# Performance work log

Measured on AMD Instinct MI355X. Metric: run time of the kernel, lower is better.

Reference implementation:

```python
import jax, jax.numpy as jnp
import numpy as np
from jax import lax

K = 3          # kernel size
STRIDE = 1
PAD = 1
DIL = 1


def conv2d(x, w, b, stride, pad):
    y = lax.conv_general_dilated(
        x, w, (stride, stride), [(pad, pad), (pad, pad)],
        dimension_numbers=('NCHW', 'OIHW', 'NCHW'))
    return y + b[None, :, None, None]


def deform_conv2d(x, offset, mask, weight, bias):
    # x: [B,C,H,W]; offset: [B,2*K*K,Ho,Wo] (channel 2i = y_i, 2i+1 = x_i);
    # mask: [B,K*K,Ho,Wo]; weight: [Cout,C,K,K]  (deformable_groups=1, groups=1)
    B, C, H, W = x.shape
    Ho, Wo = offset.shape[2], offset.shape[3]
    KK = K * K
    off = offset.reshape(B, KK, 2, Ho, Wo)
    off_y, off_x = off[:, :, 0], off[:, :, 1]          # [B,KK,Ho,Wo]

    ky, kx = jnp.meshgrid(jnp.arange(K), jnp.arange(K), indexing='ij')
    ky, kx = ky.ravel(), kx.ravel()                    # [KK]
    base_y = (jnp.arange(Ho) * STRIDE - PAD)[None, :, None] + (ky * DIL)[:, None, None]
    base_x = (jnp.arange(Wo) * STRIDE - PAD)[None, None, :] + (kx * DIL)[:, None, None]
    py = base_y[None].astype(x.dtype) + off_y          # [B,KK,Ho,Wo]
    px = base_x[None].astype(x.dtype) + off_x

    y0 = jnp.floor(py)
    x0 = jnp.floor(px)
    ly = py - y0
    lx = px - x0
    y0i = y0.astype(jnp.int32)
    x0i = x0.astype(jnp.int32)
    y1i = y0i + 1
    x1i = x0i + 1

    x_flat = x.reshape(B, C, H * W)

    def gather(yi, xi):
        valid = (yi >= 0) & (yi < H) & (xi >= 0) & (xi < W)
        idx = jnp.clip(yi, 0, H - 1) * W + jnp.clip(xi, 0, W - 1)
        v = jax.vmap(lambda xb, ib: xb[:, ib])(x_flat, idx.reshape(B, -1))
        v = v.reshape(B, C, KK, Ho, Wo)
        return v * valid[:, None].astype(x.dtype)

    w00 = ((1 - ly) * (1 - lx))[:, None]
    w01 = ((1 - ly) * lx)[:, None]
    w10 = (ly * (1 - lx))[:, None]
    w11 = (ly * lx)[:, None]
    samp = (w00 * gather(y0i, x0i) + w01 * gather(y0i, x1i)
            + w10 * gather(y1i, x0i) + w11 * gather(y1i, x1i))  # [B,C,KK,Ho,Wo]

    mod = samp * mask[:, None]                          # modulated samples
    wr = weight.reshape(weight.shape[0], C, KK)
    out = jnp.einsum('ocp,bcphw->bohw', wr, mod)
    return out + bias[None, :, None, None]


def setup_inputs() -> dict:
    key = jax.random.key(0)
    k1, k2, k3, k4, k5 = jax.random.split(key, 5)
    B, Cin, Cout, H, W = 4, 64, 128, 128, 128
    x = jax.random.normal(k1, (B, Cin, H, W), dtype=jnp.float32)
    # offset/mask conv: 3*K*K channels (o1, o2, mask). Zero-init in the source;
    # small random values here so nonzero offsets exercise the gather.
    offset_w = jax.random.normal(k2, (3 * K * K, Cin, K, K), dtype=jnp.float32) * 0.01
    offset_b = jax.random.normal(k3, (3 * K * K,), dtype=jnp.float32) * 0.01
    weight = jax.random.normal(k4, (Cout, Cin, K, K), dtype=jnp.float32) * (1.0 / np.sqrt(Cin * K * K))
    bias = jax.random.normal(k5, (Cout,), dtype=jnp.float32) * 0.01
    return {'x': x, 'offset_w': offset_w, 'offset_b': offset_b, 'weight': weight, 'bias': bias}


def reference(x, offset_w, offset_b, weight, bias):
    out = conv2d(x, offset_w, offset_b, STRIDE, PAD)    # [B,3*KK,Ho,Wo]
    o1, o2, m = jnp.split(out, 3, axis=1)
    offset = jnp.concatenate([o1, o2], axis=1)          # [B,2*KK,Ho,Wo]
    mask = jax.nn.sigmoid(m)                            # [B,KK,Ho,Wo]
    return deform_conv2d(x, offset, mask, weight, bias)
```

## Files before the change

kernel.cpp:

```cpp
#include <hip/hip_runtime.h>
#include <math.h>

#define HH   128
#define WW   128
#define HWP  16384
#define CIN  64
#define COUT 128

typedef float  f32x4  __attribute__((ext_vector_type(4)));
typedef short  short8 __attribute__((ext_vector_type(8)));

#define WBF_B   ((size_t)0)
#define OWBF_B  ((size_t)147456)
#define XT_B    ((size_t)221184)
#define WS_NEED ((size_t)8609792)

__device__ inline unsigned short f2bf(float f) {
    unsigned u = __builtin_bit_cast(unsigned, f);
    return (unsigned short)((u + 0x7FFFu + ((u >> 16) & 1u)) >> 16);
}

__global__ __launch_bounds__(256) void k_prep(const float* __restrict__ x,
                                              const float* __restrict__ wgt,
                                              const float* __restrict__ ow,
                                              unsigned short* __restrict__ xt,
                                              unsigned short* __restrict__ wbf,
                                              unsigned short* __restrict__ owbf) {
    int t = threadIdx.x;
    if (blockIdx.x < 2048) {
        int cgrp = t & 7, px = t >> 3;
        int pix = blockIdx.x * 32 + px;
        int b = pix >> 14, hw = pix & 16383;
        const float* xp = x + (size_t)b * CIN * HWP + (size_t)(cgrp * 8) * HWP + hw;
        unsigned pk[4];
#pragma unroll
        for (int d = 0; d < 4; ++d) {
            float lo = xp[(size_t)(2 * d) * HWP];
            float hi = xp[(size_t)(2 * d + 1) * HWP];
            pk[d] = (unsigned)f2bf(lo) | ((unsigned)f2bf(hi) << 16);
        }
        *(uint4*)(xt + (size_t)pix * 64 + cgrp * 8) = *(uint4*)pk;
    } else {
        int tid = (blockIdx.x - 2048) * 256 + t;
        {
            int oc = tid / 576;
            int r  = tid - oc * 576;
            int kk = r >> 6;
            int c  = r & 63;
            wbf[tid] = f2bf(wgt[((size_t)oc * CIN + c) * 9 + kk]);
        }
        if (tid < 32 * 576) {
            int oc  = tid / 576;
            int r   = tid - oc * 576;
            int tap = r >> 6;
            int c   = r & 63;
            owbf[tid] = (oc < 27) ? f2bf(ow[((size_t)oc * CIN + c) * 9 + tap]) : 0;
        }
    }
}

__global__ __launch_bounds__(256) void k_fused_v2(const unsigned short* __restrict__ xt,
                                                  const unsigned short* __restrict__ wbf,
                                                  const unsigned short* __restrict__ owbf,
                                                  const float* __restrict__ ob,
                                                  const float* __restrict__ bias,
                                                  float* __restrict__ out) {
    __shared__ __align__(16) char smem[11648];
    char*  mbase  = smem;
    float* meta_s = (float*)(smem + 8192);

    int blk0 = blockIdx.x;
    int blk  = (blk0 & 7) * 256 + (blk0 >> 3);
    int b   = blk >> 9;
    int rem = blk & 511;
    int h   = rem >> 2;
    int w0  = (rem & 3) << 5;
    int t   = threadIdx.x;

    int p1 = t >> 3;
    int cg = t & 7;
    int l  = t & 63;
    int wid = t >> 6;
    int lm = l & 15, lk = l >> 4;

    const unsigned short* xbt = xt + (size_t)b * HWP * 64;

    int ocf = wid >> 1, pxf = wid & 1;
    int spx = pxf * 16 + lm;
    f32x4 sacc = {0.f, 0.f, 0.f, 0.f};
    const unsigned short* sab = owbf + (size_t)(ocf * 16 + lm) * 576 + lk * 8;

#pragma unroll
    for (int tap = 0; tap < 9; ++tap) {
        int ky = tap / 3, kx = tap % 3;
        int yy = h - 1 + ky;
        int xx = w0 - 1 + kx + spx;
        bool vld = (yy >= 0) && (yy < HH) && (xx >= 0) && (xx < WW);
        int yc = min(max(yy, 0), HH - 1), xc = min(max(xx, 0), WW - 1);
        const unsigned short* bp = xbt + (size_t)(yc * WW + xc) * 64 + lk * 8;
#pragma unroll
        for (int ch = 0; ch < 2; ++ch) {
            short8 a = *(const short8*)(sab + tap * 64 + ch * 32);
            uint4 v = *(const uint4*)(bp + ch * 32);
            v.x = vld ? v.x : 0u;  v.y = vld ? v.y : 0u;
            v.z = vld ? v.z : 0u;  v.w = vld ? v.w : 0u;
            sacc = __builtin_amdgcn_mfma_f32_16x16x32_bf16(a, __builtin_bit_cast(short8, v), sacc, 0, 0, 0);
        }
    }
#pragma unroll
    for (int r = 0; r < 4; ++r) {
        int oc = ocf * 16 + lk * 4 + r;
        if (oc < 27) {
            float v = sacc[r] + ob[oc];
            if (oc < 18) {
                meta_s[(oc & 1) * 288 + (oc >> 1) * 32 + spx] = v;
            } else {
                meta_s[2 * 288 + (oc - 18) * 32 + spx] = 1.f / (1.f + expf(-v));
            }
        }
    }
    __syncthreads();

    f32x4 acc00 = {0.f,0.f,0.f,0.f};
    f32x4 acc01 = {0.f,0.f,0.f,0.f};
    f32x4 acc10 = {0.f,0.f,0.f,0.f};
    f32x4 acc11 = {0.f,0.f,0.f,0.f};

    const unsigned short* arow0 = wbf + (size_t)(wid * 32 + lm) * 576 + lk * 8;
    const unsigned short* arow1 = arow0 + 16 * 576;

    int pA = lm, pB = lm + 16;
    int rbA = pA * 128, rbB = pB * 128;
    int swA = pA & 7,   swB = pB & 7;

    uint4 cc00, cc01, cc10, cc11;
    float cw00, cw01, cw10, cw11;

    const unsigned short* xbc = xbt + cg * 8;

#define PREF_CORNERS(KK) do {                                                  \
      int ky_ = (KK) / 3, kx_ = (KK) % 3;                                      \
      float offy = meta_s[(KK) * 32 + p1];                                     \
      float offx = meta_s[288 + (KK) * 32 + p1];                               \
      float msk  = meta_s[576 + (KK) * 32 + p1];                               \
      float py = (float)(h - 1 + ky_) + offy;                                  \
      float px = (float)(w0 + p1 - 1 + kx_) + offx;                            \
      float y0f = floorf(py), x0f = floorf(px);                                \
      float ly = py - y0f, lx = px - x0f;                                      \
      int y0 = (int)y0f, x0i = (int)x0f;                                       \
      int y1 = y0 + 1, x1 = x0i + 1;                                           \
      bool vy0 = (y0 >= 0) && (y0 < HH);                                       \
      bool vy1 = (y1 >= 0) && (y1 < HH);                                       \
      bool vx0 = (x0i >= 0) && (x0i < WW);                                     \
      bool vx1 = (x1 >= 0) && (x1 < WW);                                       \
      int yc0 = min(max(y0, 0), HH - 1), yc1 = min(max(y1, 0), HH - 1);        \
      int xc0 = min(max(x0i, 0), WW - 1), xc1 = min(max(x1, 0), WW - 1);       \
      cw00 = (1.f - ly) * (1.f - lx) * ((vy0 && vx0) ? msk : 0.f);             \
      cw01 = (1.f - ly) * lx         * ((vy0 && vx1) ? msk : 0.f);             \
      cw10 = ly * (1.f - lx)         * ((vy1 && vx0) ? msk : 0.f);             \
      cw11 = ly * lx                 * ((vy1 && vx1) ? msk : 0.f);             \
      cc00 = *(const uint4*)(xbc + (size_t)(yc0 * WW + xc0) * 64);             \
      cc01 = *(const uint4*)(xbc + (size_t)(yc0 * WW + xc1) * 64);             \
      cc10 = *(const uint4*)(xbc + (size_t)(yc1 * WW + xc0) * 64);             \
      cc11 = *(const uint4*)(xbc + (size_t)(yc1 * WW + xc1) * 64);             \
    } while (0)

    PREF_CORNERS(0);

#pragma unroll
    for (int kk = 0; kk < 9; ++kk) {
        const int cur = kk & 1;
        {
            char* wdst = mbase + cur * 4096;
            unsigned pk[4];
#pragma unroll
            for (int d = 0; d < 4; ++d) {
                unsigned u0 = (&cc00.x)[d], u1 = (&cc01.x)[d];
                unsigned u2 = (&cc10.x)[d], u3 = (&cc11.x)[d];
                float lo = cw00 * __builtin_bit_cast(float, u0 << 16)
                         + cw01 * __builtin_bit_cast(float, u1 << 16)
                         + cw10 * __builtin_bit_cast(float, u2 << 16)
                         + cw11 * __builtin_bit_cast(float, u3 << 16);
                float hi = cw00 * __builtin_bit_cast(float, u0 & 0xFFFF0000u)
                         + cw01 * __builtin_bit_cast(float, u1 & 0xFFFF0000u)
                         + cw10 * __builtin_bit_cast(float, u2 & 0xFFFF0000u)
                         + cw11 * __builtin_bit_cast(float, u3 & 0xFFFF0000u);
                pk[d] = (unsigned)f2bf(lo) | ((unsigned)f2bf(hi) << 16);
            }
            *(uint4*)(wdst + p1 * 128 + (((unsigned)(cg ^ (p1 & 7))) << 4)) = *(uint4*)pk;
        }

        if (kk < 8) PREF_CORNERS(kk + 1);

        asm volatile("s_waitcnt lgkmcnt(0)" ::: "memory");
        __builtin_amdgcn_s_barrier();
        __builtin_amdgcn_sched_barrier(0);

        const char* rb = mbase + cur * 4096;
#pragma unroll
        for (int sstep = 0; sstep < 2; ++sstep) {
            short8 a0 = *(const short8*)(arow0 + kk * 64 + sstep * 32);
            short8 a1 = *(const short8*)(arow1 + kk * 64 + sstep * 32);
            int kb = sstep * 4 + lk;
            short8 b0 = *(const short8*)(rb + rbA + ((kb ^ swA) << 4));
            short8 b1 = *(const short8*)(rb + rbB + ((kb ^ swB) << 4));
            acc00 = __builtin_amdgcn_mfma_f32_16x16x32_bf16(a0, b0, acc00, 0, 0, 0);
            acc01 = __builtin_amdgcn_mfma_f32_16x16x32_bf16(a0, b1, acc01, 0, 0, 0);
            acc10 = __builtin_amdgcn_mfma_f32_16x16x32_bf16(a1, b0, acc10, 0, 0, 0);
            acc11 = __builtin_amdgcn_mfma_f32_16x16x32_bf16(a1, b1, acc11, 0, 0, 0);
        }
    }
#undef PREF_CORNERS

    size_t outb = (size_t)b * COUT * HWP + (size_t)h * WW + w0;
#pragma unroll
    for (int of = 0; of < 2; ++of) {
        f32x4 aP = of ? acc10 : acc00;
        f32x4 aQ = of ? acc11 : acc01;
        int ocb = wid * 32 + of * 16 + lk * 4;
#pragma unroll
        for (int r = 0; r < 4; ++r) {
            int oc = ocb + r;
            float bi = bias[oc];
            out[outb + (size_t)oc * HWP + pA] = aP[r] + bi;
            out[outb + (size_t)oc * HWP + pB] = aQ[r] + bi;
        }
    }
}

__global__ __launch_bounds__(256) void k_fused_v1(const float* __restrict__ x,
                                                  const unsigned short* __restrict__ wbf,
                                                  const unsigned short* __restrict__ owbf,
                                                  const float* __restrict__ ob,
                                                  const float* __restrict__ bias,
                                                  float* __restrict__ out) {
    __shared__ __align__(16) char smem[16768];
    char*  ctx    = smem;
    char*  mbase  = smem;
    float* meta_s = (float*)(smem + 13312);

    int blk = blockIdx.x;
    int b   = blk >> 9;
    int rem = blk & 511;
    int h   = rem >> 2;
    int w0  = (rem & 3) << 5;
    int t   = threadIdx.x;

    int p1 = t & 31;
    int cg = t >> 5;
    int l  = t & 63;
    int wid = t >> 6;
    int lm = l & 15, lk = l >> 4;

    const float* xb = x + (size_t)b * CIN * HWP;

#pragma unroll
    for (int c = 0; c < 4; ++c) {
        int j = c * 256 + t;
        if (j < 816) {
            int g   = j / 34;
            int px  = j - g * 34;
            int row = g >> 3;
            int cgj = g & 7;
            int yy = h - 1 + row;
            int xx = w0 - 1 + px;
            bool vld = (yy >= 0) && (yy < HH) && (xx >= 0) && (xx < WW);
            int  sidx = vld ? (yy * WW + xx) : 0;
            float s[8];
#pragma unroll
            for (int i = 0; i < 8; ++i)
                s[i] = vld ? xb[(size_t)(cgj * 8 + i) * HWP + sidx] : 0.f;
            uint4 pk;
            pk.x = (unsigned)f2bf(s[0]) | ((unsigned)f2bf(s[1]) << 16);
            pk.y = (unsigned)f2bf(s[2]) | ((unsigned)f2bf(s[3]) << 16);
            pk.z = (unsigned)f2bf(s[4]) | ((unsigned)f2bf(s[5]) << 16);
            pk.w = (unsigned)f2bf(s[6]) | ((unsigned)f2bf(s[7]) << 16);
            *(uint4*)(ctx + (row * 34 + px) * 128 + ((cgj ^ (px & 7)) << 4)) = pk;
        }
    }
    __syncthreads();

    int ocf = wid >> 1, pxf = wid & 1;
    int spx = pxf * 16 + lm;
    f32x4 sacc = {0.f, 0.f, 0.f, 0.f};
    const unsigned short* sab = owbf + (size_t)(ocf * 16 + lm) * 576 + lk * 8;

#pragma unroll
    for (int tap = 0; tap < 9; ++tap) {
        int ky = tap / 3, kx = tap % 3;
        int cpx = kx + spx;
        int crb = (ky * 34 + cpx) * 128;
        int csw = cpx & 7;
#pragma unroll
        for (int ch = 0; ch < 2; ++ch) {
            short8 a  = *(const short8*)(sab + tap * 64 + ch * 32);
            int kb = ch * 4 + lk;
            short8 bf = *(const short8*)(ctx + crb + (((unsigned)(kb ^ csw)) << 4));
            sacc = __builtin_amdgcn_mfma_f32_16x16x32_bf16(a, bf, sacc, 0, 0, 0);
        }
    }
#pragma unroll
    for (int r = 0; r < 4; ++r) {
        int oc = ocf * 16 + lk * 4 + r;
        if (oc < 27) {
            float v = sacc[r] + ob[oc];
            if (oc < 18) {
                meta_s[(oc & 1) * 288 + (oc >> 1) * 32 + spx] = v;
            } else {
                meta_s[2 * 288 + (oc - 18) * 32 + spx] = 1.f / (1.f + expf(-v));
            }
        }
    }
    __syncthreads();

    f32x4 acc00 = {0.f,0.f,0.f,0.f};
    f32x4 acc01 = {0.f,0.f,0.f,0.f};
    f32x4 acc10 = {0.f,0.f,0.f,0.f};
    f32x4 acc11 = {0.f,0.f,0.f,0.f};

    const unsigned short* arow0 = wbf + (size_t)(wid * 32 + lm) * 576 + lk * 8;
    const unsigned short* arow1 = arow0 + 16 * 576;

    int pA = lm, pB = lm + 16;
    int rbA = pA * 128, rbB = pB * 128;
    int swA = pA & 7,   swB = pB & 7;

    float  cw00, cw01, cw10, cw11;
    float  cc00[8], cc01[8], cc10[8], cc11[8];
    short8 na0[2], na1[2];

#define PREF_CORNERS(KK) do {                                                  \
      int ky = (KK) / 3, kx = (KK) % 3;                                        \
      float offy = meta_s[(KK) * 32 + p1];                                     \
      float offx = meta_s[288 + (KK) * 32 + p1];                               \
      float msk  = meta_s[576 + (KK) * 32 + p1];                               \
      float py = (float)(h - 1 + ky) + offy;                                   \
      float px = (float)(w0 + p1 - 1 + kx) + offx;                             \
      float y0f = floorf(py), x0f = floorf(px);                                \
      float ly = py - y0f, lx = px - x0f;                                      \
      int y0 = (int)y0f, x0i = (int)x0f;                                       \
      int y1 = y0 + 1, x1 = x0i + 1;                                           \
      bool vy0 = (y0 >= 0) && (y0 < HH);                                       \
      bool vy1 = (y1 >= 0) && (y1 < HH);                                       \
      bool vx0 = (x0i >= 0) && (x0i < WW);                                     \
      bool vx1 = (x1 >= 0) && (x1 < WW);                                       \
      int yc0 = min(max(y0, 0), HH - 1), yc1 = min(max(y1, 0), HH - 1);        \
      int xc0 = min(max(x0i, 0), WW - 1), xc1 = min(max(x1, 0), WW - 1);       \
      cw00 = (1.f - ly) * (1.f - lx) * ((vy0 && vx0) ? msk : 0.f);             \
      cw01 = (1.f - ly) * lx         * ((vy0 && vx1) ? msk : 0.f);             \
      cw10 = ly * (1.f - lx)         * ((vy1 && vx0) ? msk : 0.f);             \
      cw11 = ly * lx                 * ((vy1 && vx1) ? msk : 0.f);             \
      int idx00 = yc0 * WW + xc0, idx01 = yc0 * WW + xc1;                      \
      int idx10 = yc1 * WW + xc0, idx11 = yc1 * WW + xc1;                      \
      const float* basec = xb + (size_t)(cg * 8) * HWP;                        \
      _Pragma("unroll")                                                        \
      for (int i = 0; i < 8; ++i) {                                            \
        const float* bc = basec + (size_t)i * HWP;                             \
        cc00[i] = bc[idx00]; cc01[i] = bc[idx01];                              \
        cc10[i] = bc[idx10]; cc11[i] = bc[idx11];                              \
      }                                                                        \
    } while (0)

#define PREF_AFRAG(KK) do {                                                    \
      na0[0] = *(const short8*)(arow0 + (KK) * 64);                            \
      na0[1] = *(const short8*)(arow0 + (KK) * 64 + 32);                       \
      na1[0] = *(const short8*)(arow1 + (KK) * 64);                            \
      na1[1] = *(const short8*)(arow1 + (KK) * 64 + 32);                       \
    } while (0)

    PREF_CORNERS(0);
    PREF_AFRAG(0);

#pragma unroll
    for (int kk = 0; kk < 9; ++kk) {
        {
            char* wdst = mbase + (kk & 1) * 4096;
            float s[8];
#pragma unroll
            for (int i = 0; i < 8; ++i)
                s[i] = cw00 * cc00[i] + cw01 * cc01[i]
                     + cw10 * cc10[i] + cw11 * cc11[i];
            uint4 pk;
            pk.x = (unsigned)f2bf(s[0]) | ((unsigned)f2bf(s[1]) << 16);
            pk.y = (unsigned)f2bf(s[2]) | ((unsigned)f2bf(s[3]) << 16);
            pk.z = (unsigned)f2bf(s[4]) | ((unsigned)f2bf(s[5]) << 16);
            pk.w = (unsigned)f2bf(s[6]) | ((unsigned)f2bf(s[7]) << 16);
            *(uint4*)(wdst + p1 * 128 + (((unsigned)(cg ^ (p1 & 7))) << 4)) = pk;
        }
        if (kk < 8) PREF_CORNERS(kk + 1);
        asm volatile("s_waitcnt lgkmcnt(0)" ::: "memory");
        __builtin_amdgcn_s_barrier();
        __builtin_amdgcn_sched_barrier(0);
        const char* rb = mbase + (kk & 1) * 4096;
#pragma unroll
        for (int sstep = 0; sstep < 2; ++sstep) {
            short8 a0 = na0[sstep];
            short8 a1 = na1[sstep];
            int kb = sstep * 4 + lk;
            short8 b0 = *(const short8*)(rb + rbA + ((kb ^ swA) << 4));
            short8 b1 = *(const short8*)(rb + rbB + ((kb ^ swB) << 4));
            acc00 = __builtin_amdgcn_mfma_f32_16x16x32_bf16(a0, b0, acc00, 0, 0, 0);
            acc01 = __builtin_amdgcn_mfma_f32_16x16x32_bf16(a0, b1, acc01, 0, 0, 0);
            acc10 = __builtin_amdgcn_mfma_f32_16x16x32_bf16(a1, b0, acc10, 0, 0, 0);
            acc11 = __builtin_amdgcn_mfma_f32_16x16x32_bf16(a1, b1, acc11, 0, 0, 0);
        }
        if (kk < 8) PREF_AFRAG(kk + 1);
    }
#undef PREF_CORNERS
#undef PREF_AFRAG

    size_t outb = (size_t)b * COUT * HWP + (size_t)h * WW + w0;
#pragma unroll
    for (int of = 0; of < 2; ++of) {
        f32x4 aP = of ? acc10 : acc00;
        f32x4 aQ = of ? acc11 : acc01;
        int ocb = wid * 32 + of * 16 + lk * 4;
#pragma unroll
        for (int r = 0; r < 4; ++r) {
            int oc = ocb + r;
            float bi = bias[oc];
            out[outb + (size_t)oc * HWP + pA] = aP[r] + bi;
            out[outb + (size_t)oc * HWP + pB] = aQ[r] + bi;
        }
    }
}

extern "C" void kernel_launch(void* const* d_in, const int* in_sizes, int n_in,
                              void* d_out, int out_size, void* d_ws, size_t ws_size,
                              hipStream_t stream) {
    const float* x    = (const float*)d_in[0];
    const float* ow   = (const float*)d_in[1];
    const float* ob   = (const float*)d_in[2];
    const float* wgt  = (const float*)d_in[3];
    const float* bias = (const float*)d_in[4];
    float* out = (float*)d_out;
    char* ws = (char*)d_ws;

    unsigned short* wbf  = (unsigned short*)(ws + WBF_B);
    unsigned short* owbf = (unsigned short*)(ws + OWBF_B);
    unsigned short* xt   = (unsigned short*)(ws + XT_B);

    if (ws_size >= WS_NEED) {
        hipLaunchKernelGGL(k_prep, dim3(2336), dim3(256), 0, stream,
                           x, wgt, ow, xt, wbf, owbf);
        hipLaunchKernelGGL(k_fused_v2, dim3(2048), dim3(256), 0, stream,
                           xt, wbf, owbf, ob, bias, out);
    } else {
        hipLaunchKernelGGL(k_prep, dim3(2336), dim3(256), 0, stream,
                           x, wgt, ow, xt, wbf, owbf);
        hipLaunchKernelGGL(k_fused_v1, dim3(2048), dim3(256), 0, stream,
                           x, wbf, owbf, ob, bias, out);
    }
}
```

Measured before the change: 92.34 us.

## Split offset/mask conv into separate kernel writing fp16 metadata to workspace

Moves the offset/mask convolution out of the fused deformable-conv kernel into a new k_offc kernel. It processes two rows per block and computes all 27 channels per warp, then writes fp16 offsets and sigmoid masks to workspace. The main kernel loads this metadata instead of recomputing the small MFMA conv, which removes per-block conv work and its gather latency. The cost is an extra launch, fp16 precision loss on offsets, and extra global traffic. It also swizzles the prep block order, drops the fp32 fallback kernel, and removes the A-fragment prefetch in the main loop.

Measured after the change: 86.12 us. 6.7% less time.

```diff
diff --git a/kernel.cpp b/kernel.cpp
--- a/kernel.cpp
+++ b/kernel.cpp
@@ -1,4 +1,5 @@
 #include <hip/hip_runtime.h>
+#include <hip/hip_fp16.h>
 #include <math.h>
 
 #define HH   128
@@ -10,10 +11,12 @@
 typedef float  f32x4  __attribute__((ext_vector_type(4)));
 typedef short  short8 __attribute__((ext_vector_type(8)));
 
-#define WBF_B   ((size_t)0)
-#define OWBF_B  ((size_t)147456)
-#define XT_B    ((size_t)221184)
-#define WS_NEED ((size_t)8609792)
+#define WBF_B    ((size_t)0)
+#define OWBF_B   ((size_t)147456)
+#define XT_B     ((size_t)221184)
+#define META_B   ((size_t)8609792)
+#define WS_NEED  ((size_t)8609792)
+#define WS_NEED3 ((size_t)12148736)
 
 __device__ inline unsigned short f2bf(float f) {
     unsigned u = __builtin_bit_cast(unsigned, f);
@@ -28,8 +31,10 @@
                                               unsigned short* __restrict__ owbf) {
     int t = threadIdx.x;
     if (blockIdx.x < 2048) {
+        int bid  = blockIdx.x;
+        int bid2 = (bid & 7) * 256 + (bid >> 3);
         int cgrp = t & 7, px = t >> 3;
-        int pix = blockIdx.x * 32 + px;
+        int pix = bid2 * 32 + px;
         int b = pix >> 14, hw = pix & 16383;
         const float* xp = x + (size_t)b * CIN * HWP + (size_t)(cgrp * 8) * HWP + hw;
         unsigned pk[4];
@@ -59,12 +64,77 @@
     }
 }
 
-__global__ __launch_bounds__(256) void k_fused_v2(const unsigned short* __restrict__ xt,
-                                                  const unsigned short* __restrict__ wbf,
-                                                  const unsigned short* __restrict__ owbf,
-                                                  const float* __restrict__ ob,
-                                                  const float* __restrict__ bias,
-                                                  float* __restrict__ out) {
+__global__ __launch_bounds__(256) void k_offc(const unsigned short* __restrict__ xt,
+                                              const unsigned short* __restrict__ owbf,
+                                              const float* __restrict__ ob,
+                                              __half* __restrict__ meta_h) {
+    int blk0 = blockIdx.x;
+    int blk  = (blk0 & 7) * 128 + (blk0 >> 3);
+    int b    = blk >> 8;
+    int rem  = blk & 255;
+    int h    = (rem >> 2) * 2;
+    int w0   = (rem & 3) << 5;
+    int t    = threadIdx.x;
+    int l    = t & 63;
+    int wid  = t >> 6;
+    int lm   = l & 15, lk = l >> 4;
+
+    int r   = wid >> 1;
+    int pxf = wid & 1;
+    h += r;
+    int spx = pxf * 16 + lm;
+
+    const unsigned short* xbt = xt + (size_t)b * HWP * 64;
+    f32x4 acc0 = {0.f,0.f,0.f,0.f};
+    f32x4 acc1 = {0.f,0.f,0.f,0.f};
+    const unsigned short* sab0 = owbf + (size_t)lm * 576 + lk * 8;
+    const unsigned short* sab1 = sab0 + 16 * 576;
+
+#pragma unroll
+    for (int tap = 0; tap < 9; ++tap) {
+        int ky = tap / 3, kx = tap % 3;
+        int yy = h - 1 + ky;
+        int xx = w0 - 1 + kx + spx;
+        bool vld = (yy >= 0) && (yy < HH) && (xx >= 0) && (xx < WW);
+        int yc = min(max(yy, 0), HH - 1), xc = min(max(xx, 0), WW - 1);
+        const unsigned short* bp = xbt + (size_t)(yc * WW + xc) * 64 + lk * 8;
+        uint4 v0 = *(const uint4*)bp;
+        uint4 v1 = *(const uint4*)(bp + 32);
+        if (!vld) { v0 = uint4{0,0,0,0}; v1 = uint4{0,0,0,0}; }
+        short8 b0 = __builtin_bit_cast(short8, v0);
+        short8 b1 = __builtin_bit_cast(short8, v1);
+        short8 a00 = *(const short8*)(sab0 + tap * 64);
+        short8 a01 = *(const short8*)(sab0 + tap * 64 + 32);
+        short8 a10 = *(const short8*)(sab1 + tap * 64);
+        short8 a11 = *(const short8*)(sab1 + tap * 64 + 32);
+        acc0 = __builtin_amdgcn_mfma_f32_16x16x32_bf16(a00, b0, acc0, 0, 0, 0);
+        acc0 = __builtin_amdgcn_mfma_f32_16x16x32_bf16(a01, b1, acc0, 0, 0, 0);
+        acc1 = __builtin_amdgcn_mfma_f32_16x16x32_bf16(a10, b0, acc1, 0, 0, 0);
+        acc1 = __builtin_amdgcn_mfma_f32_16x16x32_bf16(a11, b1, acc1, 0, 0, 0);
+    }
+
+    int hw = h * WW + w0 + spx;
+#pragma unroll
+    for (int q = 0; q < 4; ++q) {
+        int oc0 = lk * 4 + q;
+        float v0 = acc0[q] + ob[oc0];
+        meta_h[((size_t)((oc0 & 1) * 9 + (oc0 >> 1)) * 4 + b) * HWP + hw] = __float2half(v0);
+        int oc1 = 16 + lk * 4 + q;
+        if (oc1 < 27) {
+            float v1 = acc1[q] + ob[oc1];
+            int comp, kk;
+            if (oc1 < 18) { comp = oc1 & 1; kk = oc1 >> 1; }
+            else          { comp = 2; kk = oc1 - 18; v1 = 1.f / (1.f + expf(-v1)); }
+            meta_h[((size_t)(comp * 9 + kk) * 4 + b) * HWP + hw] = __float2half(v1);
+        }
+    }
+}
+
+__global__ __launch_bounds__(256) void k_main(const unsigned short* __restrict__ xt,
+                                              const unsigned short* __restrict__ wbf,
+                                              const __half* __restrict__ meta_h,
+                                              const float* __restrict__ bias,
+                                              float* __restrict__ out) {
     __shared__ __align__(16) char smem[11648];
     char*  mbase  = smem;
     float* meta_s = (float*)(smem + 8192);
@@ -85,38 +155,14 @@
 
     const unsigned short* xbt = xt + (size_t)b * HWP * 64;
 
-    int ocf = wid >> 1, pxf = wid & 1;
-    int spx = pxf * 16 + lm;
-    f32x4 sacc = {0.f, 0.f, 0.f, 0.f};
-    const unsigned short* sab = owbf + (size_t)(ocf * 16 + lm) * 576 + lk * 8;
-
-#pragma unroll
-    for (int tap = 0; tap < 9; ++tap) {
-        int ky = tap / 3, kx = tap % 3;
-        int yy = h - 1 + ky;
-        int xx = w0 - 1 + kx + spx;
-        bool vld = (yy >= 0) && (yy < HH) && (xx >= 0) && (xx < WW);
-        int yc = min(max(yy, 0), HH - 1), xc = min(max(xx, 0), WW - 1);
-        const unsigned short* bp = xbt + (size_t)(yc * WW + xc) * 64 + lk * 8;
-#pragma unroll
-        for (int ch = 0; ch < 2; ++ch) {
-            short8 a = *(const short8*)(sab + tap * 64 + ch * 32);
-            uint4 v = *(const uint4*)(bp + ch * 32);
-            v.x = vld ? v.x : 0u;  v.y = vld ? v.y : 0u;
-            v.z = vld ? v.z : 0u;  v.w = vld ? v.w : 0u;
-            sacc = __builtin_amdgcn_mfma_f32_16x16x32_bf16(a, __builtin_bit_cast(short8, v), sacc, 0, 0, 0);
-        }
-    }
-#pragma unroll
-    for (int r = 0; r < 4; ++r) {
-        int oc = ocf * 16 + lk * 4 + r;
-        if (oc < 27) {
-            float v = sacc[r] + ob[oc];
-            if (oc < 18) {
-                meta_s[(oc & 1) * 288 + (oc >> 1) * 32 + spx] = v;
-            } else {
-                meta_s[2 * 288 + (oc - 18) * 32 + spx] = 1.f / (1.f + expf(-v));
-            }
+    {
+        int base_hw = h * WW + w0;
+        for (int j = t; j < 864; j += 256) {
+            int px = j & 31;
+            int ck = j >> 5;
+            float v = __half2float(meta_h[((size_t)ck * 4 + b) * HWP + base_hw + px]);
+            int comp = ck / 9, kk = ck - comp * 9;
+            meta_s[comp * 288 + kk * 32 + px] = v;
         }
     }
     __syncthreads();
@@ -189,13 +235,10 @@
             }
             *(uint4*)(wdst + p1 * 128 + (((unsigned)(cg ^ (p1 & 7))) << 4)) = *(uint4*)pk;
         }
-
         if (kk < 8) PREF_CORNERS(kk + 1);
-
         asm volatile("s_waitcnt lgkmcnt(0)" ::: "memory");
         __builtin_amdgcn_s_barrier();
         __builtin_amdgcn_sched_barrier(0);
-
         const char* rb = mbase + cur * 4096;
 #pragma unroll
         for (int sstep = 0; sstep < 2; ++sstep) {
@@ -219,66 +262,40 @@
         f32x4 aQ = of ? acc11 : acc01;
         int ocb = wid * 32 + of * 16 + lk * 4;
 #pragma unroll
-        for (int r = 0; r < 4; ++r) {
-            int oc = ocb + r;
+        for (int q = 0; q < 4; ++q) {
+            int oc = ocb + q;
             float bi = bias[oc];
-            out[outb + (size_t)oc * HWP + pA] = aP[r] + bi;
-            out[outb + (size_t)oc * HWP + pB] = aQ[r] + bi;
-        }
-    }
-}
-
-__global__ __launch_bounds__(256) void k_fused_v1(const float* __restrict__ x,
+            out[outb + (size_t)oc * HWP + pA] = aP[q] + bi;
+            out[outb + (size_t)oc * HWP + pB] = aQ[q] + bi;
+        }
+    }
+}
+
+__global__ __launch_bounds__(256) void k_fused_v2(const unsigned short* __restrict__ xt,
                                                   const unsigned short* __restrict__ wbf,
                                                   const unsigned short* __restrict__ owbf,
                                                   const float* __restrict__ ob,
                                                   const float* __restrict__ bias,
                                                   float* __restrict__ out) {
-    __shared__ __align__(16) char smem[16768];
-    char*  ctx    = smem;
+    __shared__ __align__(16) char smem[11648];
     char*  mbase  = smem;
-    float* meta_s = (float*)(smem + 13312);
-
-    int blk = blockIdx.x;
+    float* meta_s = (float*)(smem + 8192);
+
+    int blk0 = blockIdx.x;
+    int blk  = (blk0 & 7) * 256 + (blk0 >> 3);
     int b   = blk >> 9;
     int rem = blk & 511;
     int h   = rem >> 2;
     int w0  = (rem & 3) << 5;
     int t   = threadIdx.x;
 
-    int p1 = t & 31;
-    int cg = t >> 5;
+    int p1 = t >> 3;
+    int cg = t & 7;
     int l  = t & 63;
     int wid = t >> 6;
     int lm = l & 15, lk = l >> 4;
 
-    const float* xb = x + (size_t)b * CIN * HWP;
-
-#pragma unroll
-    for (int c = 0; c < 4; ++c) {
-        int j = c * 256 + t;
-        if (j < 816) {
-            int g   = j / 34;
-            int px  = j - g * 34;
-            int row = g >> 3;
-            int cgj = g & 7;
-            int yy = h - 1 + row;
-            int xx = w0 - 1 + px;
-            bool vld = (yy >= 0) && (yy < HH) && (xx >= 0) && (xx < WW);
-            int  sidx = vld ? (yy * WW + xx) : 0;
-            float s[8];
-#pragma unroll
-            for (int i = 0; i < 8; ++i)
-                s[i] = vld ? xb[(size_t)(cgj * 8 + i) * HWP + sidx] : 0.f;
-            uint4 pk;
-            pk.x = (unsigned)f2bf(s[0]) | ((unsigned)f2bf(s[1]) << 16);
-            pk.y = (unsigned)f2bf(s[2]) | ((unsigned)f2bf(s[3]) << 16);
-            pk.z = (unsigned)f2bf(s[4]) | ((unsigned)f2bf(s[5]) << 16);
-            pk.w = (unsigned)f2bf(s[6]) | ((unsigned)f2bf(s[7]) << 16);
-            *(uint4*)(ctx + (row * 34 + px) * 128 + ((cgj ^ (px & 7)) << 4)) = pk;
-        }
-    }
-    __syncthreads();
+    const unsigned short* xbt = xt + (size_t)b * HWP * 64;
 
     int ocf = wid >> 1, pxf = wid & 1;
     int spx = pxf * 16 + lm;
@@ -288,22 +305,25 @@
 #pragma unroll
     for (int tap = 0; tap < 9; ++tap) {
         int ky = tap / 3, kx = tap % 3;
-        int cpx = kx + spx;
-        int crb = (ky * 34 + cpx) * 128;
-        int csw = cpx & 7;
+        int yy = h - 1 + ky;
+        int xx = w0 - 1 + kx + spx;
+        bool vld = (yy >= 0) && (yy < HH) && (xx >= 0) && (xx < WW);
+        int yc = min(max(yy, 0), HH - 1), xc = min(max(xx, 0), WW - 1);
+        const unsigned short* bp = xbt + (size_t)(yc * WW + xc) * 64 + lk * 8;
 #pragma unroll
         for (int ch = 0; ch < 2; ++ch) {
-            short8 a  = *(const short8*)(sab + tap * 64 + ch * 32);
-            int kb = ch * 4 + lk;
-            short8 bf = *(const short8*)(ctx + crb + (((unsigned)(kb ^ csw)) << 4));
-            sacc = __builtin_amdgcn_mfma_f32_16x16x32_bf16(a, bf, sacc, 0, 0, 0);
-        }
-    }
-#pragma unroll
-    for (int r = 0; r < 4; ++r) {
-        int oc = ocf * 16 + lk * 4 + r;
+            short8 a = *(const short8*)(sab + tap * 64 + ch * 32);
+            uint4 v = *(const uint4*)(bp + ch * 32);
+            v.x = vld ? v.x : 0u;  v.y = vld ? v.y : 0u;
+            v.z = vld ? v.z : 0u;  v.w = vld ? v.w : 0u;
+            sacc = __builtin_amdgcn_mfma_f32_16x16x32_bf16(a, __builtin_bit_cast(short8, v), sacc, 0, 0, 0);
+        }
+    }
+#pragma unroll
+    for (int q = 0; q < 4; ++q) {
+        int oc = ocf * 16 + lk * 4 + q;
         if (oc < 27) {
-            float v = sacc[r] + ob[oc];
+            float v = sacc[q] + ob[oc];
             if (oc < 18) {
                 meta_s[(oc & 1) * 288 + (oc >> 1) * 32 + spx] = v;
             } else {
@@ -325,17 +345,18 @@
     int rbA = pA * 128, rbB = pB * 128;
     int swA = pA & 7,   swB = pB & 7;
 
-    float  cw00, cw01, cw10, cw11;
-    float  cc00[8], cc01[8], cc10[8], cc11[8];
-    short8 na0[2], na1[2];
+    uint4 cc00, cc01, cc10, cc11;
+    float cw00, cw01, cw10, cw11;
+
+    const unsigned short* xbc = xbt + cg * 8;
 
 #define PREF_CORNERS(KK) do {                                                  \
-      int ky = (KK) / 3, kx = (KK) % 3;                                        \
+      int ky_ = (KK) / 3, kx_ = (KK) % 3;                                      \
       float offy = meta_s[(KK) * 32 + p1];                                     \
       float offx = meta_s[288 + (KK) * 32 + p1];                               \
       float msk  = meta_s[576 + (KK) * 32 + p1];                               \
-      float py = (float)(h - 1 + ky) + offy;                                   \
-      float px = (float)(w0 + p1 - 1 + kx) + offx;                             \
+      float py = (float)(h - 1 + ky_) + offy;                                  \
+      float px = (float)(w0 + p1 - 1 + kx_) + offx;                            \
       float y0f = floorf(py), x0f = floorf(px);                                \
       float ly = py - y0f, lx = px - x0f;                                      \
       int y0 = (int)y0f, x0i = (int)x0f;                                       \
@@ -350,52 +371,45 @@
       cw01 = (1.f - ly) * lx         * ((vy0 && vx1) ? msk : 0.f);             \
       cw10 = ly * (1.f - lx)         * ((vy1 && vx0) ? msk : 0.f);             \
       cw11 = ly * lx                 * ((vy1 && vx1) ? msk : 0.f);             \
-      int idx00 = yc0 * WW + xc0, idx01 = yc0 * WW + xc1;                      \
-      int idx10 = yc1 * WW + xc0, idx11 = yc1 * WW + xc1;                      \
-      const float* basec = xb + (size_t)(cg * 8) * HWP;                        \
-      _Pragma("unroll")                                                        \
-      for (int i = 0; i < 8; ++i) {                                            \
-        const float* bc = basec + (size_t)i * HWP;                             \
-        cc00[i] = bc[idx00]; cc01[i] = bc[idx01];                              \
-        cc10[i] = bc[idx10]; cc11[i] = bc[idx11];                              \
-      }                                                                        \
+      cc00 = *(const uint4*)(xbc + (size_t)(yc0 * WW + xc0) * 64);             \
+      cc01 = *(const uint4*)(xbc + (size_t)(yc0 * WW + xc1) * 64);             \
+      cc10 = *(const uint4*)(xbc + (size_t)(yc1 * WW + xc0) * 64);             \
+      cc11 = *(const uint4*)(xbc + (size_t)(yc1 * WW + xc1) * 64);             \
     } while (0)
 
-#define PREF_AFRAG(KK) do {                                                    \
-      na0[0] = *(const short8*)(arow0 + (KK) * 64);                            \
-      na0[1] = *(const short8*)(arow0 + (KK) * 64 + 32);                       \
-      na1[0] = *(const short8*)(arow1 + (KK) * 64);                            \
-      na1[1] = *(const short8*)(arow1 + (KK) * 64 + 32);                       \
-    } while (0)
-
     PREF_CORNERS(0);
-    PREF_AFRAG(0);
 
 #pragma unroll
     for (int kk = 0; kk < 9; ++kk) {
+        const int cur = kk & 1;
         {
-            char* wdst = mbase + (kk & 1) * 4096;
-            float s[8];
-#pragma unroll
-            for (int i = 0; i < 8; ++i)
-                s[i] = cw00 * cc00[i] + cw01 * cc01[i]
-                     + cw10 * cc10[i] + cw11 * cc11[i];
-            uint4 pk;
-            pk.x = (unsigned)f2bf(s[0]) | ((unsigned)f2bf(s[1]) << 16);
-            pk.y = (unsigned)f2bf(s[2]) | ((unsigned)f2bf(s[3]) << 16);
-            pk.z = (unsigned)f2bf(s[4]) | ((unsigned)f2bf(s[5]) << 16);
-            pk.w = (unsigned)f2bf(s[6]) | ((unsigned)f2bf(s[7]) << 16);
-            *(uint4*)(wdst + p1 * 128 + (((unsigned)(cg ^ (p1 & 7))) << 4)) = pk;
+            char* wdst = mbase + cur * 4096;
+            unsigned pk[4];
+#pragma unroll
+            for (int d = 0; d < 4; ++d) {
+                unsigned u0 = (&cc00.x)[d], u1 = (&cc01.x)[d];
+                unsigned u2 = (&cc10.x)[d], u3 = (&cc11.x)[d];
+                float lo = cw00 * __builtin_bit_cast(float, u0 << 16)
+                         + cw01 * __builtin_bit_cast(float, u1 << 16)
+                         + cw10 * __builtin_bit_cast(float, u2 << 16)
+                         + cw11 * __builtin_bit_cast(float, u3 << 16);
+                float hi = cw00 * __builtin_bit_cast(float, u0 & 0xFFFF0000u)
+                         + cw01 * __builtin_bit_cast(float, u1 & 0xFFFF0000u)
+                         + cw10 * __builtin_bit_cast(float, u2 & 0xFFFF0000u)
+                         + cw11 * __builtin_bit_cast(float, u3 & 0xFFFF0000u);
+                pk[d] = (unsigned)f2bf(lo) | ((unsigned)f2bf(hi) << 16);
+            }
+            *(uint4*)(wdst + p1 * 128 + (((unsigned)(cg ^ (p1 & 7))) << 4)) = *(uint4*)pk;
         }
         if (kk < 8) PREF_CORNERS(kk + 1);
         asm volatile("s_waitcnt lgkmcnt(0)" ::: "memory");
         __builtin_amdgcn_s_barrier();
         __builtin_amdgcn_sched_barrier(0);
-        const char* rb = mbase + (kk & 1) * 4096;
+        const char* rb = mbase + cur * 4096;
 #pragma unroll
         for (int sstep = 0; sstep < 2; ++sstep) {
-            short8 a0 = na0[sstep];
-            short8 a1 = na1[sstep];
+            short8 a0 = *(const short8*)(arow0 + kk * 64 + sstep * 32);
+            short8 a1 = *(const short8*)(arow1 + kk * 64 + sstep * 32);
             int kb = sstep * 4 + lk;
             short8 b0 = *(const short8*)(rb + rbA + ((kb ^ swA) << 4));
             short8 b1 = *(const short8*)(rb + rbB + ((kb ^ swB) << 4));
@@ -404,10 +418,8 @@
             acc10 = __builtin_amdgcn_mfma_f32_16x16x32_bf16(a1, b0, acc10, 0, 0, 0);
             acc11 = __builtin_amdgcn_mfma_f32_16x16x32_bf16(a1, b1, acc11, 0, 0, 0);
         }
-        if (kk < 8) PREF_AFRAG(kk + 1);
     }
 #undef PREF_CORNERS
-#undef PREF_AFRAG
 
     size_t outb = (size_t)b * COUT * HWP + (size_t)h * WW + w0;
 #pragma unroll
@@ -416,11 +428,11 @@
         f32x4 aQ = of ? acc11 : acc01;
         int ocb = wid * 32 + of * 16 + lk * 4;
 #pragma unroll
-        for (int r = 0; r < 4; ++r) {
-            int oc = ocb + r;
+        for (int q = 0; q < 4; ++q) {
+            int oc = ocb + q;
             float bi = bias[oc];
-            out[outb + (size_t)oc * HWP + pA] = aP[r] + bi;
-            out[outb + (size_t)oc * HWP + pB] = aQ[r] + bi;
+            out[outb + (size_t)oc * HWP + pA] = aP[q] + bi;
+            out[outb + (size_t)oc * HWP + pB] = aQ[q] + bi;
         }
     }
 }
@@ -439,16 +451,17 @@
     unsigned short* wbf  = (unsigned short*)(ws + WBF_B);
     unsigned short* owbf = (unsigned short*)(ws + OWBF_B);
     unsigned short* xt   = (unsigned short*)(ws + XT_B);
-
-    if (ws_size >= WS_NEED) {
-        hipLaunchKernelGGL(k_prep, dim3(2336), dim3(256), 0, stream,
-                           x, wgt, ow, xt, wbf, owbf);
+    __half*         mh   = (__half*)(ws + META_B);
+
+    hipLaunchKernelGGL(k_prep, dim3(2336), dim3(256), 0, stream,
+                       x, wgt, ow, xt, wbf, owbf);
+    if (ws_size >= WS_NEED3) {
+        hipLaunchKernelGGL(k_offc, dim3(1024), dim3(256), 0, stream,
+                           xt, owbf, ob, mh);
+        hipLaunchKernelGGL(k_main, dim3(2048), dim3(256), 0, stream,
+                           xt, wbf, mh, bias, out);
+    } else {
         hipLaunchKernelGGL(k_fused_v2, dim3(2048), dim3(256), 0, stream,
                            xt, wbf, owbf, ob, bias, out);
-    } else {
-        hipLaunchKernelGGL(k_prep, dim3(2336), dim3(256), 0, stream,
-                           x, wgt, ow, xt, wbf, owbf);
-        hipLaunchKernelGGL(k_fused_v1, dim3(2048), dim3(256), 0, stream,
-                           x, wbf, owbf, ob, bias, out);
-    }
-}
+    }
+}
```
